# Optimization experiments

Measured on AMD Instinct MI355X. Metric: run time of the kernel, lower is better.

## Reference

```python
import jax, jax.numpy as jnp
import numpy as np

NUM_NODES = 2048
EMB = (512, 512, 256)
LATENT = 512
N_FEAT = 512
N_TOTAL = 16384  # batch_size * NUM_NODES
N_EDGES = 524288


def setup_inputs() -> dict:
    key = jax.random.key(0)
    ks = jax.random.split(key, 14)
    s = 0.02
    inp = {
        "x": jax.random.normal(ks[0], (N_TOTAL, N_FEAT), jnp.float32),
        "edge_index": jax.random.randint(ks[1], (2, N_EDGES), 0, N_TOTAL, dtype=jnp.int64),
        "batch_size": 8,
        "batch_index": jax.random.randint(ks[2], (N_TOTAL,), 0, 8, dtype=jnp.int64),
        "W1": jax.random.normal(ks[3], (N_FEAT, EMB[0]), jnp.float32) * s,
        "b1": jnp.zeros((EMB[0],), jnp.float32),
        "W2": jax.random.normal(ks[4], (EMB[0], EMB[1]), jnp.float32) * s,
        "b2": jnp.zeros((EMB[1],), jnp.float32),
        "W3": jax.random.normal(ks[5], (EMB[1], EMB[2]), jnp.float32) * s,
        "b3": jnp.zeros((EMB[2],), jnp.float32),
        "We": jax.random.normal(ks[6], (NUM_NODES * EMB[2], LATENT), jnp.float32) * s,
        "be": jnp.zeros((LATENT,), jnp.float32),
        "Wd": jax.random.normal(ks[7], (LATENT, NUM_NODES), jnp.float32) * s,
        "bd": jnp.zeros((NUM_NODES,), jnp.float32),
    }
    return inp


def reference(x, edge_index, batch_size, batch_index, W1, b1, W2, b2, W3, b3, We, be, Wd, bd):
    N = x.shape[0]
    loops = jnp.arange(N)
    row = jnp.concatenate([edge_index[0], loops])  # sources
    col = jnp.concatenate([edge_index[1], loops])  # targets
    # symmetric degree normalization (PyG GCNConv with self loops)
    deg = jax.ops.segment_sum(jnp.ones_like(col, dtype=x.dtype), col, num_segments=N)
    dinv = jnp.where(deg > 0, jax.lax.rsqrt(deg), jnp.zeros_like(deg))
    norm = (dinv[row] * dinv[col])[:, None]  # [E+N, 1]

    def gcn(h, W, b):
        h = h @ W  # transform first (PyG order)
        return jax.ops.segment_sum(h[row] * norm, col, num_segments=N) + b

    h = jax.nn.relu(gcn(x, W1, b1))
    h = jax.nn.relu(gcn(h, W2, b2))
    h = gcn(h, W3, b3)                      # [N, EMB[2]]
    h = h.reshape(-1, NUM_NODES * EMB[2])   # [batch, NUM_NODES*EMB[2]]
    z = h @ We + be                          # encoder Linear
    out = z @ Wd + bd                        # decoder Linear -> [batch, NUM_NODES]
    return out
```

## Files before the change

kernel.cpp:

```cpp
#include <hip/hip_runtime.h>
#include <stdint.h>

#define NT 16384
#define NN 2048
#define NB 8
#define NBKT 16

typedef __attribute__((ext_vector_type(4))) float f32x4;
typedef __attribute__((ext_vector_type(2))) float f32x2;
typedef __attribute__((ext_vector_type(8))) short s16x8;
typedef __attribute__((ext_vector_type(4))) short s16x4;

__device__ __forceinline__ float bf2f(short u) {
    unsigned v = ((unsigned)(unsigned short)u) << 16;
    return __builtin_bit_cast(float, v);
}
__device__ __forceinline__ short f2bf(float f) {
    unsigned u = __builtin_bit_cast(unsigned, f);
    u += 0x7fffu + ((u >> 16) & 1u);
    return (short)(u >> 16);
}
__device__ __forceinline__ void gload16(const void* g, void* l) {
    __builtin_amdgcn_global_load_lds(
        (const __attribute__((address_space(1))) void*)g,
        (__attribute__((address_space(3))) void*)l, 16, 0, 0);
}
__device__ __forceinline__ long long eidx(const void* ei, long long i, int is64) {
    if (is64) return ((const long long*)ei)[i];
    return (long long)((const int*)ei)[i];
}

__global__ void k_detect(const void* ei, int nchk, int* flag) {
    __shared__ int bad;
    if (threadIdx.x == 0) bad = 0;
    __syncthreads();
    const long long* p = (const long long*)ei;
    for (int i = threadIdx.x; i < nchk; i += 256) {
        long long v = p[i];
        if (v < 0 || v >= NT) bad = 1;
    }
    __syncthreads();
    if (threadIdx.x == 0) *flag = bad ? 0 : 1;
}

__global__ void k_count16(const void* ei, int E, const int* flag, int* cnt16) {
    int e = blockIdx.x * 256 + threadIdx.x;
    if (e >= E) return;
    int f = *flag;
    int r = (int)eidx(ei, e, f);
    int c = (int)eidx(ei, (long long)E + e, f);
    atomicAdd(&cnt16[c * NBKT + (r >> 10)], 1);
}

__global__ void k_deg(const int* __restrict__ cnt16, int* __restrict__ deg) {
    int n = blockIdx.x * 256 + threadIdx.x;
    const int* p = cnt16 + n * NBKT;
    int s = 0;
#pragma unroll
    for (int j = 0; j < NBKT; j++) s += p[j];
    deg[n] = s;
}

__global__ __launch_bounds__(1024) void k_scan(const int* __restrict__ count,
        int* __restrict__ offs, float* __restrict__ dinv) {
    __shared__ int ps[1024];
    const int t = threadIdx.x;
    const int base = t * 16;
    int loc[16];
    int s = 0;
#pragma unroll
    for (int j = 0; j < 16; j++) { loc[j] = count[base + j]; s += loc[j]; }
    ps[t] = s;
    __syncthreads();
    for (int o = 1; o < 1024; o <<= 1) {
        int v = (t >= o) ? ps[t - o] : 0;
        __syncthreads();
        ps[t] += v;
        __syncthreads();
    }
    int ex = ps[t] - s;
#pragma unroll
    for (int j = 0; j < 16; j++) {
        offs[base + j] = ex;
        ex += loc[j];
        dinv[base + j] = rsqrtf((float)(loc[j] + 1));
    }
}

__global__ void k_bcur(const int* __restrict__ cnt16, const int* __restrict__ offs,
                       int* __restrict__ bcur) {
    int n = blockIdx.x * 256 + threadIdx.x;
    int running = offs[n];
#pragma unroll
    for (int b = 0; b < NBKT; b++) {
        bcur[n * NBKT + b] = running;
        running += cnt16[n * NBKT + b];
    }
}

__global__ void k_fill16(const void* ei, int E, const int* flag,
                         int* bcur, int* csr) {
    int e = blockIdx.x * 256 + threadIdx.x;
    if (e >= E) return;
    int f = *flag;
    int r = (int)eidx(ei, e, f);
    int c = (int)eidx(ei, (long long)E + e, f);
    int pos = atomicAdd(&bcur[c * NBKT + (r >> 10)], 1);
    csr[pos] = r;
}

__global__ void k_convw_all(const float* __restrict__ W1, const float* __restrict__ W2,
                            const float* __restrict__ W3, short* __restrict__ Wt1,
                            short* __restrict__ Wt2, short* __restrict__ Wt3) {
    int idx = blockIdx.x * 256 + threadIdx.x;
    const float* W; short* Wt; int N, base;
    if (idx < 262144)      { W = W1; Wt = Wt1; N = 512; base = idx; }
    else if (idx < 524288) { W = W2; Wt = Wt2; N = 512; base = idx - 262144; }
    else                   { W = W3; Wt = Wt3; N = 256; base = idx - 524288; }
    int k = base / N, n = base - k * N;
    Wt[(size_t)n * 512 + k] = f2bf(W[base]);
}

__global__ __launch_bounds__(256) void k_scale_x(const float* __restrict__ x,
        const float* __restrict__ dinv, short* __restrict__ xs) {
    int i = blockIdx.x * 256 + threadIdx.x;
    f32x4 v = *(const f32x4*)(x + (size_t)i * 4);
    float d = dinv[i >> 7];
    s16x4 o;
#pragma unroll
    for (int j = 0; j < 4; j++) o[j] = f2bf(v[j] * d);
    *(s16x4*)(xs + (size_t)i * 4) = o;
}

__global__ __launch_bounds__(256, 4) void k_gemm(const short* __restrict__ A,
        const short* __restrict__ Bt, short* __restrict__ Co, int N, int K) {
    __shared__ short As[64 * 64];
    __shared__ short Bs[128 * 64];
    const int t = threadIdx.x;
    const int w = t >> 6, l = t & 63;
    const int row0 = blockIdx.x * 64;
    const int col0 = blockIdx.y * 128;
    const int lr = l & 15, lhi = l >> 4;
    const int wc = w * 32;
    f32x4 acc[4][2] = {};
    int arow[2], ajs[2], brow[4], bjs[4];
#pragma unroll
    for (int i = 0; i < 2; i++) {
        int s = t + i * 256;
        arow[i] = s >> 3; ajs[i] = (s & 7) ^ (arow[i] & 7);
    }
#pragma unroll
    for (int i = 0; i < 4; i++) {
        int s = t + i * 256;
        brow[i] = s >> 3; bjs[i] = (s & 7) ^ (brow[i] & 7);
    }
    int aoff[2][4], boff[2][2];
#pragma unroll
    for (int kk = 0; kk < 2; kk++) {
#pragma unroll
        for (int m = 0; m < 4; m++) {
            int ar = m * 16 + lr;
            aoff[kk][m] = ar * 64 + (((kk * 4 + lhi) ^ (ar & 7)) << 3);
        }
#pragma unroll
        for (int n = 0; n < 2; n++) {
            int br = wc + n * 16 + lr;
            boff[kk][n] = br * 64 + (((kk * 4 + lhi) ^ (br & 7)) << 3);
        }
    }
    for (int k0 = 0; k0 < K; k0 += 64) {
#pragma unroll
        for (int i = 0; i < 2; i++)
            gload16(A + (size_t)(row0 + arow[i]) * K + k0 + ajs[i] * 8,
                    (void*)(As + (t + i * 256) * 8));
#pragma unroll
        for (int i = 0; i < 4; i++)
            gload16(Bt + (size_t)(col0 + brow[i]) * K + k0 + bjs[i] * 8,
                    (void*)(Bs + (t + i * 256) * 8));
        __syncthreads();
#pragma unroll
        for (int kk = 0; kk < 2; kk++) {
            s16x8 af[4], bfr[2];
#pragma unroll
            for (int m = 0; m < 4; m++) af[m]  = *(const s16x8*)(As + aoff[kk][m]);
#pragma unroll
            for (int n = 0; n < 2; n++) bfr[n] = *(const s16x8*)(Bs + boff[kk][n]);
#pragma unroll
            for (int m = 0; m < 4; m++)
#pragma unroll
                for (int n = 0; n < 2; n++)
                    acc[m][n] = __builtin_amdgcn_mfma_f32_16x16x32_bf16(af[m], bfr[n], acc[m][n], 0, 0, 0);
        }
        __syncthreads();
    }
#pragma unroll
    for (int m = 0; m < 4; m++)
#pragma unroll
        for (int n = 0; n < 2; n++)
#pragma unroll
            for (int j = 0; j < 4; j++) {
                int r = row0 + m * 16 + lhi * 4 + j;
                int c = col0 + wc + n * 16 + lr;
                Co[(size_t)r * N + c] = f2bf(acc[m][n][j]);
            }
}

__global__ __launch_bounds__(256) void k_agg512(const short* __restrict__ T,
        const int* __restrict__ offs, const int* __restrict__ cnt,
        const int* __restrict__ csr, const float* __restrict__ dinv,
        const float* __restrict__ bias, short* __restrict__ H) {
    const int w = threadIdx.x >> 6, l = threadIdx.x & 63;
    const int node = blockIdx.x * 4 + w;
    const int c0 = l * 8;
    const short* base = T + c0;
    float acc[8];
    {
        s16x8 r = *(const s16x8*)(base + (size_t)node * 512);
#pragma unroll
        for (int v = 0; v < 8; v++) acc[v] = bf2f(r[v]);
    }
    const int beg = offs[node], end = beg + cnt[node];
    int j = beg;
    for (; j + 8 <= end; j += 8) {
        int sIx[8];
#pragma unroll
        for (int q = 0; q < 8; q++) sIx[q] = csr[j + q];
        s16x8 r[8];
#pragma unroll
        for (int q = 0; q < 8; q++) r[q] = *(const s16x8*)(base + (size_t)sIx[q] * 512);
#pragma unroll
        for (int v = 0; v < 8; v++) {
            float s01 = bf2f(r[0][v]) + bf2f(r[1][v]);
            float s23 = bf2f(r[2][v]) + bf2f(r[3][v]);
            float s45 = bf2f(r[4][v]) + bf2f(r[5][v]);
            float s67 = bf2f(r[6][v]) + bf2f(r[7][v]);
            acc[v] += (s01 + s23) + (s45 + s67);
        }
    }
    for (; j + 2 <= end; j += 2) {
        int s0 = csr[j], s1 = csr[j + 1];
        s16x8 r0 = *(const s16x8*)(base + (size_t)s0 * 512);
        s16x8 r1 = *(const s16x8*)(base + (size_t)s1 * 512);
#pragma unroll
        for (int v = 0; v < 8; v++) acc[v] += bf2f(r0[v]) + bf2f(r1[v]);
    }
    for (; j < end; j++) {
        s16x8 r0 = *(const s16x8*)(base + (size_t)csr[j] * 512);
#pragma unroll
        for (int v = 0; v < 8; v++) acc[v] += bf2f(r0[v]);
    }
    const float dc = dinv[node];
    f32x4 b0 = *(const f32x4*)(bias + c0);
    f32x4 b1 = *(const f32x4*)(bias + c0 + 4);
    s16x8 outv;
#pragma unroll
    for (int v = 0; v < 8; v++) {
        float bb = (v < 4) ? b0[v] : b1[v - 4];
        float o = acc[v] * dc + bb;
        o = fmaxf(o, 0.f);
        o *= dc;
        outv[v] = f2bf(o);
    }
    *(s16x8*)(H + (size_t)node * 512 + c0) = outv;
}

__global__ __launch_bounds__(256) void k_agg256(const short* __restrict__ T,
        const int* __restrict__ offs, const int* __restrict__ cnt,
        const int* __restrict__ csr, const float* __restrict__ dinv,
        const float* __restrict__ bias, float* __restrict__ H3) {
    const int w = threadIdx.x >> 6, l = threadIdx.x & 63;
    const int node = blockIdx.x * 4 + w;
    const int c0 = l * 4;
    const short* base = T + c0;
    float acc[4];
    {
        s16x4 r = *(const s16x4*)(base + (size_t)node * 256);
#pragma unroll
        for (int v = 0; v < 4; v++) acc[v] = bf2f(r[v]);
    }
    const int beg = offs[node], end = beg + cnt[node];
    int j = beg;
    for (; j + 8 <= end; j += 8) {
        int sIx[8];
#pragma unroll
        for (int q = 0; q < 8; q++) sIx[q] = csr[j + q];
        s16x4 r[8];
#pragma unroll
        for (int q = 0; q < 8; q++) r[q] = *(const s16x4*)(base + (size_t)sIx[q] * 256);
#pragma unroll
        for (int v = 0; v < 4; v++) {
            float s01 = bf2f(r[0][v]) + bf2f(r[1][v]);
            float s23 = bf2f(r[2][v]) + bf2f(r[3][v]);
            float s45 = bf2f(r[4][v]) + bf2f(r[5][v]);
            float s67 = bf2f(r[6][v]) + bf2f(r[7][v]);
            acc[v] += (s01 + s23) + (s45 + s67);
        }
    }
    for (; j < end; j++) {
        s16x4 r0 = *(const s16x4*)(base + (size_t)csr[j] * 256);
#pragma unroll
        for (int v = 0; v < 4; v++) acc[v] += bf2f(r0[v]);
    }
    const float dc = dinv[node];
    f32x4 bb = *(const f32x4*)(bias + c0);
    f32x4 o;
#pragma unroll
    for (int v = 0; v < 4; v++) o[v] = acc[v] * dc + bb[v];
    *(f32x4*)(H3 + (size_t)node * 256 + c0) = o;
}

__global__ __launch_bounds__(256) void k_enc(const float* __restrict__ h3,
        const float* __restrict__ We, float* __restrict__ part) {
    __shared__ float hT[512 * 8];
    __shared__ float red[32 * 128];
    const int t = threadIdx.x;
    const int k0 = blockIdx.x * 512;
    for (int i = t; i < 4096; i += 256) {
        int b = i >> 9, k = i & 511;
        hT[k * 8 + b] = h3[(size_t)b * 524288 + k0 + k];
    }
    __syncthreads();
    const int col = (t & 127) * 4;
    const int khalf = t >> 7;
    float acc[8][4] = {};
    const float* wp = We + (size_t)(k0 + khalf * 256) * 512 + col;
    const float* hp = hT + khalf * 256 * 8;
#pragma unroll 2
    for (int k = 0; k < 256; k++) {
        f32x4 wv = *(const f32x4*)(wp + (size_t)k * 512);
        f32x4 ha = *(const f32x4*)(hp + k * 8);
        f32x4 hb = *(const f32x4*)(hp + k * 8 + 4);
#pragma unroll
        for (int c = 0; c < 4; c++) {
            acc[0][c] += ha[0] * wv[c];
            acc[1][c] += ha[1] * wv[c];
            acc[2][c] += ha[2] * wv[c];
            acc[3][c] += ha[3] * wv[c];
            acc[4][c] += hb[0] * wv[c];
            acc[5][c] += hb[1] * wv[c];
            acc[6][c] += hb[2] * wv[c];
            acc[7][c] += hb[3] * wv[c];
        }
    }
    if (khalf) {
#pragma unroll
        for (int b = 0; b < 8; b++)
#pragma unroll
            for (int c = 0; c < 4; c++)
                red[(b * 4 + c) * 128 + (t - 128)] = acc[b][c];
    }
    __syncthreads();
    if (!khalf) {
#pragma unroll
        for (int b = 0; b < 8; b++) {
            f32x4 o;
#pragma unroll
            for (int c = 0; c < 4; c++) o[c] = acc[b][c] + red[(b * 4 + c) * 128 + t];
            *(f32x4*)(part + (size_t)blockIdx.x * 4096 + b * 512 + col) = o;
        }
    }
}

__global__ __launch_bounds__(256) void k_zred(const float* __restrict__ part,
                                              float* __restrict__ zpart) {
    const int n = blockIdx.x * 256 + threadIdx.x;
    const int p0 = blockIdx.y * 128;
    float s = 0.f;
    for (int q = 0; q < 128; q++) s += part[(size_t)(p0 + q) * 4096 + n];
    zpart[(size_t)blockIdx.y * 4096 + n] = s;
}

__global__ __launch_bounds__(256) void k_dec(const float* __restrict__ zpart,
        const float* __restrict__ be, const float* __restrict__ Wd,
        const float* __restrict__ bd, float* __restrict__ out) {
    __shared__ float zs[512];
    const int b = blockIdx.x >> 3;
    const int n = ((blockIdx.x & 7) << 8) + threadIdx.x;
    for (int i = threadIdx.x; i < 512; i += 256) {
        float s = be[i];
#pragma unroll
        for (int p = 0; p < 8; p++) s += zpart[(size_t)p * 4096 + b * 512 + i];
        zs[i] = s;
    }
    __syncthreads();
    float acc = bd[n];
    for (int k = 0; k < 512; k++) acc += zs[k] * Wd[(size_t)k * 2048 + n];
    out[b * 2048 + n] = acc;
}

extern "C" void kernel_launch(void* const* d_in, const int* in_sizes, int n_in,
                              void* d_out, int out_size, void* d_ws, size_t ws_size,
                              hipStream_t stream) {
    const float* x  = (const float*)d_in[0];
    const void*  ei = d_in[1];
    const float* W1 = (const float*)d_in[4];
    const float* b1 = (const float*)d_in[5];
    const float* W2 = (const float*)d_in[6];
    const float* b2 = (const float*)d_in[7];
    const float* W3 = (const float*)d_in[8];
    const float* b3 = (const float*)d_in[9];
    const float* We = (const float*)d_in[10];
    const float* be = (const float*)d_in[11];
    const float* Wd = (const float*)d_in[12];
    const float* bd = (const float*)d_in[13];
    float* out = (float*)d_out;
    const int E = in_sizes[1] / 2;

    char* ws = (char*)d_ws;
    size_t off = 0;
    auto alloc = [&](size_t bytes) {
        void* p = ws + off;
        off = (off + bytes + 255) & ~(size_t)255;
        return p;
    };
    int*   flag   = (int*)  alloc(4);
    int*   deg    = (int*)  alloc((size_t)NT * 4);
    int*   offs   = (int*)  alloc((size_t)NT * 4);
    float* dinv   = (float*)alloc((size_t)NT * 4);
    int*   csr    = (int*)  alloc((size_t)E * 4);
    short* Wt1    = (short*)alloc((size_t)512 * 512 * 2);
    short* Wt2    = (short*)alloc((size_t)512 * 512 * 2);
    short* Wt3    = (short*)alloc((size_t)256 * 512 * 2);
    short* bufA   = (short*)alloc((size_t)NT * 512 * 2);
    short* bufB   = (short*)alloc((size_t)NT * 512 * 2);
    float* part   = (float*)alloc((size_t)1024 * 4096 * 4);
    float* zpart  = (float*)alloc((size_t)8 * 4096 * 4);
    int*   cnt16  = (int*)part;
    int*   bcur   = ((int*)part) + NT * NBKT;

    hipMemsetAsync(cnt16, 0, (size_t)NT * NBKT * 4, stream);

    k_detect<<<1, 256, 0, stream>>>(ei, 2048, flag);
    k_count16<<<(E + 255) / 256, 256, 0, stream>>>(ei, E, flag, cnt16);
    k_deg<<<NT / 256, 256, 0, stream>>>(cnt16, deg);
    k_scan<<<1, 1024, 0, stream>>>(deg, offs, dinv);
    k_bcur<<<NT / 256, 256, 0, stream>>>(cnt16, offs, bcur);
    k_fill16<<<(E + 255) / 256, 256, 0, stream>>>(ei, E, flag, bcur, csr);

    k_convw_all<<<2560, 256, 0, stream>>>(W1, W2, W3, Wt1, Wt2, Wt3);
    k_scale_x<<<(NT * 512 / 4) / 256, 256, 0, stream>>>(x, dinv, bufA);

    dim3 g1(256, 4);
    k_gemm<<<g1, 256, 0, stream>>>(bufA, Wt1, bufB, 512, 512);
    k_agg512<<<NT / 4, 256, 0, stream>>>(bufB, offs, deg, csr, dinv, b1, bufA);
    k_gemm<<<g1, 256, 0, stream>>>(bufA, Wt2, bufB, 512, 512);
    k_agg512<<<NT / 4, 256, 0, stream>>>(bufB, offs, deg, csr, dinv, b2, bufA);
    dim3 g3(256, 2);
    k_gemm<<<g3, 256, 0, stream>>>(bufA, Wt3, bufB, 256, 512);
    k_agg256<<<NT / 4, 256, 0, stream>>>(bufB, offs, deg, csr, dinv, b3, (float*)bufA);

    k_enc<<<1024, 256, 0, stream>>>((const float*)bufA, We, part);
    dim3 gz(16, 8);
    k_zred<<<gz, 256, 0, stream>>>(part, zpart);
    k_dec<<<64, 256, 0, stream>>>(zpart, be, Wd, bd, out);
}
```

Before: 505.5 us.

## Fuse layer-3 aggregation into encoder GEMM and merge small setup kernels

The final GCN aggregation (k_agg256) is folded into the encoder kernel. Each block aggregates the 2 local nodes across all 8 batches that its 512-wide K slice needs, writes them to shared memory, and then runs the We product. This removes the fp32 H3 round trip through global memory and one launch. The memset and the edge-index detect kernel are also merged into one init kernel, and the x scaling and weight conversion are merged into one launch. The cost is that the gather now sits serially ahead of the We streaming inside each block, with only 1024 blocks available to hide the gather latency.

Measured after the change: 493.2 us. 2.4% less time.

```diff
diff --git a/kernel.cpp b/kernel.cpp
--- a/kernel.cpp
+++ b/kernel.cpp
@@ -7,7 +7,6 @@
 #define NBKT 16
 
 typedef __attribute__((ext_vector_type(4))) float f32x4;
-typedef __attribute__((ext_vector_type(2))) float f32x2;
 typedef __attribute__((ext_vector_type(8))) short s16x8;
 typedef __attribute__((ext_vector_type(4))) short s16x4;
 
@@ -30,17 +29,23 @@
     return (long long)((const int*)ei)[i];
 }
 
-__global__ void k_detect(const void* ei, int nchk, int* flag) {
-    __shared__ int bad;
-    if (threadIdx.x == 0) bad = 0;
-    __syncthreads();
-    const long long* p = (const long long*)ei;
-    for (int i = threadIdx.x; i < nchk; i += 256) {
-        long long v = p[i];
-        if (v < 0 || v >= NT) bad = 1;
-    }
-    __syncthreads();
-    if (threadIdx.x == 0) *flag = bad ? 0 : 1;
+__global__ void k_init(const void* ei, int* flag, int* cnt16) {
+    if (blockIdx.x == 64) {
+        __shared__ int bad;
+        if (threadIdx.x == 0) bad = 0;
+        __syncthreads();
+        const long long* p = (const long long*)ei;
+        for (int i = threadIdx.x; i < 2048; i += 256) {
+            long long v = p[i];
+            if (v < 0 || v >= NT) bad = 1;
+        }
+        __syncthreads();
+        if (threadIdx.x == 0) *flag = bad ? 0 : 1;
+    } else {
+        int base = blockIdx.x * 4096 + threadIdx.x;
+#pragma unroll
+        for (int q = 0; q < 16; q++) cnt16[base + q * 256] = 0;
+    }
 }
 
 __global__ void k_count16(const void* ei, int E, const int* flag, int* cnt16) {
@@ -109,27 +114,28 @@
     csr[pos] = r;
 }
 
-__global__ void k_convw_all(const float* __restrict__ W1, const float* __restrict__ W2,
+__global__ void k_convscale(const float* __restrict__ W1, const float* __restrict__ W2,
                             const float* __restrict__ W3, short* __restrict__ Wt1,
-                            short* __restrict__ Wt2, short* __restrict__ Wt3) {
-    int idx = blockIdx.x * 256 + threadIdx.x;
-    const float* W; short* Wt; int N, base;
-    if (idx < 262144)      { W = W1; Wt = Wt1; N = 512; base = idx; }
-    else if (idx < 524288) { W = W2; Wt = Wt2; N = 512; base = idx - 262144; }
-    else                   { W = W3; Wt = Wt3; N = 256; base = idx - 524288; }
-    int k = base / N, n = base - k * N;
-    Wt[(size_t)n * 512 + k] = f2bf(W[base]);
-}
-
-__global__ __launch_bounds__(256) void k_scale_x(const float* __restrict__ x,
-        const float* __restrict__ dinv, short* __restrict__ xs) {
-    int i = blockIdx.x * 256 + threadIdx.x;
-    f32x4 v = *(const f32x4*)(x + (size_t)i * 4);
-    float d = dinv[i >> 7];
-    s16x4 o;
-#pragma unroll
-    for (int j = 0; j < 4; j++) o[j] = f2bf(v[j] * d);
-    *(s16x4*)(xs + (size_t)i * 4) = o;
+                            short* __restrict__ Wt2, short* __restrict__ Wt3,
+                            const float* __restrict__ x, const float* __restrict__ dinv,
+                            short* __restrict__ xs) {
+    if (blockIdx.x < 8192) {
+        int i = blockIdx.x * 256 + threadIdx.x;
+        f32x4 v = *(const f32x4*)(x + (size_t)i * 4);
+        float d = dinv[i >> 7];
+        s16x4 o;
+#pragma unroll
+        for (int j = 0; j < 4; j++) o[j] = f2bf(v[j] * d);
+        *(s16x4*)(xs + (size_t)i * 4) = o;
+    } else {
+        int idx = (blockIdx.x - 8192) * 256 + threadIdx.x;
+        const float* W; short* Wt; int N, base;
+        if (idx < 262144)      { W = W1; Wt = Wt1; N = 512; base = idx; }
+        else if (idx < 524288) { W = W2; Wt = Wt2; N = 512; base = idx - 262144; }
+        else                   { W = W3; Wt = Wt3; N = 256; base = idx - 524288; }
+        int k = base / N, n = base - k * N;
+        Wt[(size_t)n * 512 + k] = f2bf(W[base]);
+    }
 }
 
 __global__ __launch_bounds__(256, 4) void k_gemm(const short* __restrict__ A,
@@ -264,82 +270,79 @@
     *(s16x8*)(H + (size_t)node * 512 + c0) = outv;
 }
 
-__global__ __launch_bounds__(256) void k_agg256(const short* __restrict__ T,
+__global__ __launch_bounds__(256) void k_enc(const short* __restrict__ T,
         const int* __restrict__ offs, const int* __restrict__ cnt,
         const int* __restrict__ csr, const float* __restrict__ dinv,
-        const float* __restrict__ bias, float* __restrict__ H3) {
-    const int w = threadIdx.x >> 6, l = threadIdx.x & 63;
-    const int node = blockIdx.x * 4 + w;
+        const float* __restrict__ b3, const float* __restrict__ We,
+        float* __restrict__ part) {
+    __shared__ float hB[8 * 512];
+    __shared__ float red[32 * 128];
+    const int t = threadIdx.x;
+    const int w = t >> 6, l = t & 63;
+    const int ln0 = blockIdx.x * 2;
     const int c0 = l * 4;
     const short* base = T + c0;
-    float acc[4];
-    {
-        s16x4 r = *(const s16x4*)(base + (size_t)node * 256);
-#pragma unroll
-        for (int v = 0; v < 4; v++) acc[v] = bf2f(r[v]);
-    }
-    const int beg = offs[node], end = beg + cnt[node];
-    int j = beg;
-    for (; j + 8 <= end; j += 8) {
-        int sIx[8];
-#pragma unroll
-        for (int q = 0; q < 8; q++) sIx[q] = csr[j + q];
-        s16x4 r[8];
-#pragma unroll
-        for (int q = 0; q < 8; q++) r[q] = *(const s16x4*)(base + (size_t)sIx[q] * 256);
-#pragma unroll
-        for (int v = 0; v < 4; v++) {
-            float s01 = bf2f(r[0][v]) + bf2f(r[1][v]);
-            float s23 = bf2f(r[2][v]) + bf2f(r[3][v]);
-            float s45 = bf2f(r[4][v]) + bf2f(r[5][v]);
-            float s67 = bf2f(r[6][v]) + bf2f(r[7][v]);
-            acc[v] += (s01 + s23) + (s45 + s67);
-        }
-    }
-    for (; j < end; j++) {
-        s16x4 r0 = *(const s16x4*)(base + (size_t)csr[j] * 256);
-#pragma unroll
-        for (int v = 0; v < 4; v++) acc[v] += bf2f(r0[v]);
-    }
-    const float dc = dinv[node];
-    f32x4 bb = *(const f32x4*)(bias + c0);
-    f32x4 o;
-#pragma unroll
-    for (int v = 0; v < 4; v++) o[v] = acc[v] * dc + bb[v];
-    *(f32x4*)(H3 + (size_t)node * 256 + c0) = o;
-}
-
-__global__ __launch_bounds__(256) void k_enc(const float* __restrict__ h3,
-        const float* __restrict__ We, float* __restrict__ part) {
-    __shared__ float hT[512 * 8];
-    __shared__ float red[32 * 128];
-    const int t = threadIdx.x;
-    const int k0 = blockIdx.x * 512;
-    for (int i = t; i < 4096; i += 256) {
-        int b = i >> 9, k = i & 511;
-        hT[k * 8 + b] = h3[(size_t)b * 524288 + k0 + k];
+    f32x4 bb = *(const f32x4*)(b3 + c0);
+    for (int p = 0; p < 4; p++) {
+        const int i = w * 4 + p;
+        const int b = i >> 1, lnk = i & 1;
+        const int node = b * NN + ln0 + lnk;
+        float acc[4];
+        {
+            s16x4 r = *(const s16x4*)(base + (size_t)node * 256);
+#pragma unroll
+            for (int v = 0; v < 4; v++) acc[v] = bf2f(r[v]);
+        }
+        const int beg = offs[node], end = beg + cnt[node];
+        int j = beg;
+        for (; j + 8 <= end; j += 8) {
+            int sIx[8];
+#pragma unroll
+            for (int q = 0; q < 8; q++) sIx[q] = csr[j + q];
+            s16x4 r[8];
+#pragma unroll
+            for (int q = 0; q < 8; q++) r[q] = *(const s16x4*)(base + (size_t)sIx[q] * 256);
+#pragma unroll
+            for (int v = 0; v < 4; v++) {
+                float s01 = bf2f(r[0][v]) + bf2f(r[1][v]);
+                float s23 = bf2f(r[2][v]) + bf2f(r[3][v]);
+                float s45 = bf2f(r[4][v]) + bf2f(r[5][v]);
+                float s67 = bf2f(r[6][v]) + bf2f(r[7][v]);
+                acc[v] += (s01 + s23) + (s45 + s67);
+            }
+        }
+        for (; j < end; j++) {
+            s16x4 r0 = *(const s16x4*)(base + (size_t)csr[j] * 256);
+#pragma unroll
+            for (int v = 0; v < 4; v++) acc[v] += bf2f(r0[v]);
+        }
+        const float dc = dinv[node];
+        f32x4 o;
+#pragma unroll
+        for (int v = 0; v < 4; v++) o[v] = acc[v] * dc + bb[v];
+        *(f32x4*)(&hB[b * 512 + lnk * 256 + c0]) = o;
     }
     __syncthreads();
     const int col = (t & 127) * 4;
     const int khalf = t >> 7;
     float acc[8][4] = {};
-    const float* wp = We + (size_t)(k0 + khalf * 256) * 512 + col;
-    const float* hp = hT + khalf * 256 * 8;
+    const float* wp = We + (size_t)(blockIdx.x * 512 + khalf * 256) * 512 + col;
+    const float* hp = hB + khalf * 256;
 #pragma unroll 2
     for (int k = 0; k < 256; k++) {
         f32x4 wv = *(const f32x4*)(wp + (size_t)k * 512);
-        f32x4 ha = *(const f32x4*)(hp + k * 8);
-        f32x4 hb = *(const f32x4*)(hp + k * 8 + 4);
+        float h0 = hp[k],        h1 = hp[512 + k],  h2 = hp[1024 + k], h3v = hp[1536 + k];
+        float h4 = hp[2048 + k], h5 = hp[2560 + k], h6 = hp[3072 + k], h7 = hp[3584 + k];
 #pragma unroll
         for (int c = 0; c < 4; c++) {
-            acc[0][c] += ha[0] * wv[c];
-            acc[1][c] += ha[1] * wv[c];
-            acc[2][c] += ha[2] * wv[c];
-            acc[3][c] += ha[3] * wv[c];
-            acc[4][c] += hb[0] * wv[c];
-            acc[5][c] += hb[1] * wv[c];
-            acc[6][c] += hb[2] * wv[c];
-            acc[7][c] += hb[3] * wv[c];
+            acc[0][c] += h0 * wv[c];
+            acc[1][c] += h1 * wv[c];
+            acc[2][c] += h2 * wv[c];
+            acc[3][c] += h3v * wv[c];
+            acc[4][c] += h4 * wv[c];
+            acc[5][c] += h5 * wv[c];
+            acc[6][c] += h6 * wv[c];
+            acc[7][c] += h7 * wv[c];
         }
     }
     if (khalf) {
@@ -428,17 +431,14 @@
     int*   cnt16  = (int*)part;
     int*   bcur   = ((int*)part) + NT * NBKT;
 
-    hipMemsetAsync(cnt16, 0, (size_t)NT * NBKT * 4, stream);
-
-    k_detect<<<1, 256, 0, stream>>>(ei, 2048, flag);
+    k_init<<<65, 256, 0, stream>>>(ei, flag, cnt16);
     k_count16<<<(E + 255) / 256, 256, 0, stream>>>(ei, E, flag, cnt16);
     k_deg<<<NT / 256, 256, 0, stream>>>(cnt16, deg);
     k_scan<<<1, 1024, 0, stream>>>(deg, offs, dinv);
     k_bcur<<<NT / 256, 256, 0, stream>>>(cnt16, offs, bcur);
     k_fill16<<<(E + 255) / 256, 256, 0, stream>>>(ei, E, flag, bcur, csr);
 
-    k_convw_all<<<2560, 256, 0, stream>>>(W1, W2, W3, Wt1, Wt2, Wt3);
-    k_scale_x<<<(NT * 512 / 4) / 256, 256, 0, stream>>>(x, dinv, bufA);
+    k_convscale<<<10752, 256, 0, stream>>>(W1, W2, W3, Wt1, Wt2, Wt3, x, dinv, bufA);
 
     dim3 g1(256, 4);
     k_gemm<<<g1, 256, 0, stream>>>(bufA, Wt1, bufB, 512, 512);
@@ -447,9 +447,8 @@
     k_agg512<<<NT / 4, 256, 0, stream>>>(bufB, offs, deg, csr, dinv, b2, bufA);
     dim3 g3(256, 2);
     k_gemm<<<g3, 256, 0, stream>>>(bufA, Wt3, bufB, 256, 512);
-    k_agg256<<<NT / 4, 256, 0, stream>>>(bufB, offs, deg, csr, dinv, b3, (float*)bufA);
-
-    k_enc<<<1024, 256, 0, stream>>>((const float*)bufA, We, part);
+
+    k_enc<<<1024, 256, 0, stream>>>(bufB, offs, deg, csr, dinv, b3, We, part);
     dim3 gz(16, 8);
     k_zred<<<gz, 256, 0, stream>>>(part, zpart);
     k_dec<<<64, 256, 0, stream>>>(zpart, be, Wd, bd, out);
```
